# Kernel optimization log

Measured on AMD Instinct MI355X. Metric: run time of the kernel, lower is better.

The kernel has to match this reference:

```python
import jax, jax.numpy as jnp
import numpy as np
from jax import lax

B, LATENT, HIDDEN, N_STEPS = 2048, 256, 512, 100


def setup_inputs() -> dict:
    key = jax.random.key(0)
    ks = jax.random.split(key, 9)
    s_ih = 1.0 / np.sqrt(HIDDEN)
    return {
        "p0": jax.random.normal(ks[0], (B, LATENT), jnp.float32),
        "lat": jax.random.uniform(ks[1], (B,), jnp.float32, -1.0, 1.0),
        "lon": jax.random.uniform(ks[2], (B,), jnp.float32, -1.0, 1.0),
        "W_ih": jax.random.normal(ks[3], (3 * HIDDEN, LATENT + 2), jnp.float32) * s_ih,
        "W_hh": jax.random.normal(ks[4], (3 * HIDDEN, HIDDEN), jnp.float32) * s_ih,
        "b_ih": jax.random.normal(ks[5], (3 * HIDDEN,), jnp.float32) * s_ih,
        "b_hh": jax.random.normal(ks[6], (3 * HIDDEN,), jnp.float32) * s_ih,
        "W_proj": jax.random.normal(ks[7], (LATENT, HIDDEN), jnp.float32) * s_ih,
        "b_proj": jax.random.normal(ks[8], (LATENT,), jnp.float32) * s_ih,
        "n_steps": N_STEPS,
    }


def reference(p0, lat, lon, W_ih, W_hh, b_ih, b_hh, W_proj, b_proj, n_steps):
    H = W_hh.shape[1]
    ll = jnp.stack([lat, lon], axis=-1)  # (B, 2) conditioning, constant per step

    def step(carry, _):
        p, h = carry
        x = jnp.concatenate([p, ll], axis=-1)          # (B, latent+2)
        gi = x @ W_ih.T + b_ih                          # (B, 3H)
        gh = h @ W_hh.T + b_hh                          # (B, 3H)
        i_r, i_z, i_n = jnp.split(gi, 3, axis=-1)       # PyTorch gate order r,z,n
        h_r, h_z, h_n = jnp.split(gh, 3, axis=-1)
        r = jax.nn.sigmoid(i_r + h_r)
        z = jax.nn.sigmoid(i_z + h_z)
        n = jnp.tanh(i_n + r * h_n)
        h_new = (1.0 - z) * n + z * h
        p_new = h_new @ W_proj.T + b_proj               # (B, latent)
        return (p_new, h_new), p_new

    h0 = jnp.zeros((p0.shape[0], H), p0.dtype)
    _, ps = lax.scan(step, (p0, h0), None, length=n_steps)  # (T-1, B, latent)
    return jnp.concatenate([p0[None], ps], axis=0)          # (T, B, latent)
```

## Files before the change

kernel.cpp:

```cpp
#include <hip/hip_runtime.h>
#include <math.h>


#define B_SZ 2048
#define LAT  256
#define HID  512
#define NROW 2304
#define HN   (B_SZ * HID)

typedef unsigned short u16;
typedef __attribute__((ext_vector_type(4))) short s16x4;
typedef __attribute__((ext_vector_type(8))) short s16x8;
typedef __attribute__((ext_vector_type(4))) float f32x4;

__device__ __forceinline__ float sigm(float x) { return 1.0f / (1.0f + __expf(-x)); }
__device__ __forceinline__ float tanh_f(float x) {
    float e = __expf(-2.0f * fabsf(x));
    float t = (1.0f - e) / (1.0f + e);
    return copysignf(t, x);
}
__device__ __forceinline__ u16 f2bf(float x) {
    unsigned u = __float_as_uint(x);
    return (u16)((u + 0x7FFFu + ((u >> 16) & 1u)) >> 16);
}
__device__ __forceinline__ float bf2f(u16 h) { return __uint_as_float((unsigned)h << 16); }

__device__ __forceinline__ size_t fidx(int n, int k) {
    return ((size_t)(n >> 4) * 16 + (k >> 5)) * 512 +
           (size_t)((k >> 3) & 3) * 128 + (n & 15) * 8 + (k & 7);
}

__global__ __launch_bounds__(64) void k_bias(
    const float* __restrict__ W_ih, const float* __restrict__ b_ih,
    const float* __restrict__ b_hh, const float* __restrict__ b_pr,
    float* __restrict__ Bias)
{
    const int u = blockIdx.x;
    const int t = threadIdx.x;
    float dr = 0.f, dz = 0.f, dn = 0.f;
    for (int o = t; o < 256; o += 64) {
        float bo = b_pr[o];
        dr = fmaf(bo, W_ih[(size_t)u * 258 + o], dr);
        dz = fmaf(bo, W_ih[(size_t)(HID + u) * 258 + o], dz);
        dn = fmaf(bo, W_ih[(size_t)(2 * HID + u) * 258 + o], dn);
    }
    #pragma unroll
    for (int off = 32; off > 0; off >>= 1) {
        dr += __shfl_down(dr, off);
        dz += __shfl_down(dz, off);
        dn += __shfl_down(dn, off);
    }
    if (t == 0) {
        float* b = Bias + u * 12;
        b[0]  = b_ih[u] + b_hh[u] + dr;
        b[1]  = W_ih[(size_t)u * 258 + 256];
        b[2]  = W_ih[(size_t)u * 258 + 257];
        b[3]  = b_ih[HID + u] + b_hh[HID + u] + dz;
        b[4]  = W_ih[(size_t)(HID + u) * 258 + 256];
        b[5]  = W_ih[(size_t)(HID + u) * 258 + 257];
        b[6]  = b_ih[2 * HID + u] + dn;
        b[7]  = W_ih[(size_t)(2 * HID + u) * 258 + 256];
        b[8]  = W_ih[(size_t)(2 * HID + u) * 258 + 257];
        b[9]  = b_hh[2 * HID + u];
        b[10] = b_hh[u];
        b[11] = b_hh[HID + u];
    }
}

__global__ __launch_bounds__(512) void k_gi1(
    const float* __restrict__ p0, const float* __restrict__ latv,
    const float* __restrict__ lonv, const float* __restrict__ W_ih,
    const float* __restrict__ b_ih, float* __restrict__ gi1T,
    float* __restrict__ out)
{
    const int rb = blockIdx.x;
    const int t  = threadIdx.x;
    __shared__ float p0s[8][256];
    __shared__ float lat_s[8], lon_s[8];
    for (int i = t; i < 8 * 256; i += 512) {
        int r = i >> 8, o = i & 255;
        float v = p0[(size_t)(rb * 8 + r) * LAT + o];
        p0s[r][o] = v;
        out[(size_t)(rb * 8 + r) * LAT + o] = v;
    }
    if (t < 8) { lat_s[t] = latv[rb * 8 + t]; lon_s[t] = lonv[rb * 8 + t]; }
    __syncthreads();

    for (int gg = 0; gg < 3; ++gg) {
        const int grow = t + gg * 512;
        const float* wr = W_ih + (size_t)grow * 258;
        float acc[8];
        float bi = b_ih[grow];
        #pragma unroll
        for (int r = 0; r < 8; ++r) acc[r] = bi;
        for (int o = 0; o < 256; ++o) {
            float wv = wr[o];
            #pragma unroll
            for (int r = 0; r < 8; ++r) acc[r] = fmaf(wv, p0s[r][o], acc[r]);
        }
        float c1 = wr[256], c2 = wr[257];
        #pragma unroll
        for (int r = 0; r < 8; ++r) {
            acc[r] = fmaf(lat_s[r], c1, acc[r]);
            acc[r] = fmaf(lon_s[r], c2, acc[r]);
            gi1T[(size_t)grow * B_SZ + rb * 8 + r] = acc[r];
        }
    }
}

__global__ __launch_bounds__(256) void k_h1(
    const float* __restrict__ gi1T, const float* __restrict__ Bias,
    u16* __restrict__ Hhi, u16* __restrict__ Hlo)
{
    const int idx = blockIdx.x * 256 + threadIdx.x;
    const int row = idx & (B_SZ - 1);
    const int u   = idx >> 11;
    const float* bb = Bias + (size_t)u * 12;
    float r = sigm(gi1T[(size_t)u * B_SZ + row] + bb[10]);
    float z = sigm(gi1T[(size_t)(HID + u) * B_SZ + row] + bb[11]);
    float n = tanh_f(fmaf(r, bb[9], gi1T[(size_t)(2 * HID + u) * B_SZ + row]));
    float h = n - z * n;
    u16 hi = f2bf(h);
    size_t off = HN + fidx(row, u);
    Hhi[off] = hi;
    Hlo[off] = f2bf(h - bf2f(hi));
}

__global__ __launch_bounds__(512) void k_wsplit(
    const float* __restrict__ W_ih, const float* __restrict__ W_hh,
    const float* __restrict__ W_pr, u16* __restrict__ Whi, u16* __restrict__ Wlo)
{
    const int n = blockIdx.x;
    const int k = threadIdx.x;
    const int u = n >> 2, g = n & 3;
    __shared__ float wr[256];
    if (n < 2048 && g != 3 && k < 256)
        wr[k] = W_ih[(size_t)(g * HID + u) * 258 + k];
    __syncthreads();

    float w;
    if (n >= 2048) {
        w = W_pr[(size_t)(n - 2048) * HID + k];
    } else if (g == 3) {
        w = W_hh[(size_t)(2 * HID + u) * HID + k];
    } else {
        float acc = 0.f;
        for (int o = 0; o < 256; ++o)
            acc = fmaf(wr[o], W_pr[(size_t)o * HID + k], acc);
        if (g == 0)      acc += W_hh[(size_t)u * HID + k];
        else if (g == 1) acc += W_hh[(size_t)(HID + u) * HID + k];
        w = acc;
    }
    u16 hi = f2bf(w);
    size_t off = fidx(n, k);
    Whi[off] = hi;
    Wlo[off] = f2bf(w - bf2f(hi));
}

__global__ __launch_bounds__(256, 4) void k_gates(
    u16* __restrict__ Hhi, u16* __restrict__ Hlo,
    const u16* __restrict__ Whi,
    const float* __restrict__ Bias,
    const float* __restrict__ latv, const float* __restrict__ lonv,
    int sA, int sW, int ra, int rw)
{
    const int bid = blockIdx.x;
    const int xcd = bid & 7, loc = bid >> 3;
    const int mt  = (xcd & 3) * 8 + (loc & 7);
    const int nt  = (xcd >> 2) * 16 + (loc >> 3);
    const int m0  = mt * 64, n0 = nt * 64;
    const int t    = threadIdx.x;
    const int lane = t & 63, wave = t >> 6;
    const int wm   = wave >> 1, wn = wave & 1;
    const int q    = lane >> 4, c = lane & 15;

    __shared__ float Gt[64][68];
    __shared__ float bias_s[16][12];
    if (t < 192) ((float*)bias_s)[t] = Bias[(size_t)(n0 >> 2) * 12 + t];

    const u16* __restrict__ Hh = Hhi + (size_t)sA * HN;
    const u16* __restrict__ Hl = Hlo + (size_t)ra * HN;

    int aoff[2], boff[2];
    #pragma unroll
    for (int i = 0; i < 2; ++i)
        aoff[i] = ((mt * 4 + wm * 2 + i) * 16) * 512 + lane * 8;
    #pragma unroll
    for (int j = 0; j < 2; ++j)
        boff[j] = ((nt * 4 + wn * 2 + j) * 16) * 512 + lane * 8;

    f32x4 acc[2][2];
    #pragma unroll
    for (int i = 0; i < 2; ++i)
        #pragma unroll
        for (int j = 0; j < 2; ++j) acc[i][j] = (f32x4){0.f, 0.f, 0.f, 0.f};

    #pragma unroll 2
    for (int kb = 0; kb < 16; ++kb) {
        const int ko = kb * 512;
        s16x8 ah[2], bh[2];
        #pragma unroll
        for (int i = 0; i < 2; ++i)
            ah[i] = *(const s16x8*)(Hh + aoff[i] + ko);
        #pragma unroll
        for (int j = 0; j < 2; ++j)
            bh[j] = *(const s16x8*)(Whi + boff[j] + ko);
        #pragma unroll
        for (int i = 0; i < 2; ++i)
            #pragma unroll
            for (int j = 0; j < 2; ++j)
                acc[i][j] = __builtin_amdgcn_mfma_f32_16x16x32_bf16(ah[i], bh[j], acc[i][j], 0, 0, 0);
    }

    #pragma unroll
    for (int i = 0; i < 2; ++i)
        #pragma unroll
        for (int j = 0; j < 2; ++j)
            #pragma unroll
            for (int r = 0; r < 4; ++r)
                Gt[wm * 32 + i * 16 + 4 * q + r][wn * 32 + j * 16 + c] = acc[i][j][r];
    __syncthreads();

    u16* __restrict__ Hhn = Hhi + (size_t)sW * HN;
    u16* __restrict__ Hln = Hlo + (size_t)rw * HN;

    const int ug = t & 3;
    const int ml = t >> 2;
    const int m  = m0 + ml;
    const float lt = latv[m], ln = lonv[m];
    const size_t hoff = ((size_t)(m >> 4) * 16 + (nt >> 1)) * 512 +
                        (size_t)((nt & 1) * 2 + (ug >> 1)) * 128 +
                        (m & 15) * 8 + (ug & 1) * 4;
    s16x4 hh4 = *(const s16x4*)(Hh + hoff);
    s16x4 hl4 = *(const s16x4*)(Hl + hoff);
    s16x4 vh, vl;
    #pragma unroll
    for (int j = 0; j < 4; ++j) {
        const float* bb = bias_s[ug * 4 + j];
        f32x4 gv = *(const f32x4*)&Gt[ml][(ug * 4 + j) * 4];
        float r = sigm(gv.x + bb[0] + lt * bb[1] + ln * bb[2]);
        float z = sigm(gv.y + bb[3] + lt * bb[4] + ln * bb[5]);
        float n = tanh_f(fmaf(r, gv.w + bb[9], gv.z + bb[6] + lt * bb[7] + ln * bb[8]));
        float hold = bf2f((u16)hh4[j]) + bf2f((u16)hl4[j]);
        float h = n + z * (hold - n);
        u16 hi = f2bf(h);
        vh[j] = (short)hi;
        vl[j] = (short)f2bf(h - bf2f(hi));
    }
    *(s16x4*)(Hhn + hoff) = vh;
    *(s16x4*)(Hln + hoff) = vl;
}

__global__ __launch_bounds__(256, 2) void k_proj(
    const u16* __restrict__ Hhi, const u16* __restrict__ Whi,
    const float* __restrict__ b_pr, float* __restrict__ out)
{
    const int bid  = blockIdx.x;
    const int pt   = bid >> 1, ntp = bid & 1;
    const int slab = (pt >> 4) + 1;
    const int mt   = pt & 15;
    const int m0   = mt * 128;
    const int t    = threadIdx.x;
    const int lane = t & 63, wave = t >> 6;
    const int wm   = wave >> 1, wn = wave & 1;
    const int q    = lane >> 4, c = lane & 15;

    __shared__ float Gt[64][132];

    const u16* __restrict__ Hh = Hhi + (size_t)slab * HN;

    int aoff[4], boff[4];
    #pragma unroll
    for (int i = 0; i < 4; ++i) {
        aoff[i] = ((mt * 8 + wm * 4 + i) * 16) * 512 + lane * 8;
        boff[i] = ((128 + ntp * 8 + wn * 4 + i) * 16) * 512 + lane * 8;
    }

    f32x4 acc[4][4];
    #pragma unroll
    for (int i = 0; i < 4; ++i)
        #pragma unroll
        for (int j = 0; j < 4; ++j) acc[i][j] = (f32x4){0.f, 0.f, 0.f, 0.f};

    #pragma unroll 2
    for (int kb = 0; kb < 16; ++kb) {
        const int ko = kb * 512;
        s16x8 ah[4], bh[4];
        #pragma unroll
        for (int i = 0; i < 4; ++i) {
            ah[i] = *(const s16x8*)(Hh  + aoff[i] + ko);
            bh[i] = *(const s16x8*)(Whi + boff[i] + ko);
        }
        #pragma unroll
        for (int i = 0; i < 4; ++i)
            #pragma unroll
            for (int j = 0; j < 4; ++j)
                acc[i][j] = __builtin_amdgcn_mfma_f32_16x16x32_bf16(ah[i], bh[j], acc[i][j], 0, 0, 0);
    }

    for (int half = 0; half < 2; ++half) {
        __syncthreads();
        if (wm == half) {
            #pragma unroll
            for (int i = 0; i < 4; ++i)
                #pragma unroll
                for (int j = 0; j < 4; ++j)
                    #pragma unroll
                    for (int r = 0; r < 4; ++r)
                        Gt[i * 16 + 4 * q + r][wn * 64 + j * 16 + c] = acc[i][j][r];
        }
        __syncthreads();

        const int cl = t & 31, rg = t >> 5;
        const int o  = ntp * 128 + cl * 4;
        const float4 bp = *(const float4*)(b_pr + o);
        float* ob = out + (size_t)slab * B_SZ * LAT + o;
        #pragma unroll
        for (int i = 0; i < 8; ++i) {
            const int ml2 = rg * 8 + i;
            f32x4 g = *(const f32x4*)&Gt[ml2][cl * 4];
            *(float4*)(ob + (size_t)(m0 + half * 64 + ml2) * LAT) =
                make_float4(g.x + bp.x, g.y + bp.y, g.z + bp.z, g.w + bp.w);
        }
    }
}

__global__ __launch_bounds__(256) void k_gemm(
    u16* __restrict__ Hhi, u16* __restrict__ Hlo,
    const u16* __restrict__ Whi, const u16* __restrict__ Wlo,
    const float* __restrict__ Bias, const float* __restrict__ b_pr,
    const float* __restrict__ latv, const float* __restrict__ lonv,
    float* __restrict__ out, int s, int ns, int ntb, int ntc)
{
    const int bid  = blockIdx.x;
    const int nt   = ntb + bid % ntc;
    const int mt   = bid / ntc;
    const int m0   = mt * 128, n0 = nt * 128;
    const int t    = threadIdx.x;
    const int lane = t & 63, wave = t >> 6;
    const int wm   = wave >> 1, wn = wave & 1;
    const int q    = lane >> 4, c = lane & 15;

    __shared__ float Gt[64][132];
    __shared__ float bias_s[32][12];
    if (n0 < 2048) {
        for (int i = t; i < 384; i += 256)
            ((float*)bias_s)[i] = Bias[(size_t)(n0 >> 2) * 12 + i];
    }

    const u16* __restrict__ Hh = Hhi + (size_t)((s - 1) & 1) * HN;
    const u16* __restrict__ Hl = Hlo + (size_t)((s - 1) & 1) * HN;

    int aoff[4], boff[4];
    #pragma unroll
    for (int i = 0; i < 4; ++i) {
        aoff[i] = ((mt * 8 + wm * 4 + i) * 16) * 512 + lane * 8;
        boff[i] = ((nt * 8 + wn * 4 + i) * 16) * 512 + lane * 8;
    }

    f32x4 acc[4][4];
    #pragma unroll
    for (int i = 0; i < 4; ++i)
        #pragma unroll
        for (int j = 0; j < 4; ++j) acc[i][j] = (f32x4){0.f, 0.f, 0.f, 0.f};

    #pragma unroll 2
    for (int kb = 0; kb < 16; ++kb) {
        const int ko = kb * 512;
        s16x8 ah[4], al[4], bh[4], bl[4];
        #pragma unroll
        for (int i = 0; i < 4; ++i) {
            ah[i] = *(const s16x8*)(Hh  + aoff[i] + ko);
            al[i] = *(const s16x8*)(Hl  + aoff[i] + ko);
            bh[i] = *(const s16x8*)(Whi + boff[i] + ko);
            bl[i] = *(const s16x8*)(Wlo + boff[i] + ko);
        }
        #pragma unroll
        for (int i = 0; i < 4; ++i)
            #pragma unroll
            for (int j = 0; j < 4; ++j) {
                acc[i][j] = __builtin_amdgcn_mfma_f32_16x16x32_bf16(ah[i], bh[j], acc[i][j], 0, 0, 0);
                acc[i][j] = __builtin_amdgcn_mfma_f32_16x16x32_bf16(al[i], bh[j], acc[i][j], 0, 0, 0);
                acc[i][j] = __builtin_amdgcn_mfma_f32_16x16x32_bf16(ah[i], bl[j], acc[i][j], 0, 0, 0);
            }
    }

    u16* __restrict__ Hhn = Hhi + (size_t)(s & 1) * HN;
    u16* __restrict__ Hln = Hlo + (size_t)(s & 1) * HN;
    const int u0t = n0 >> 2;

    for (int half = 0; half < 2; ++half) {
        __syncthreads();
        if (wm == half) {
            #pragma unroll
            for (int i = 0; i < 4; ++i)
                #pragma unroll
                for (int j = 0; j < 4; ++j)
                    #pragma unroll
                    for (int r = 0; r < 4; ++r)
                        Gt[i * 16 + 4 * q + r][wn * 64 + j * 16 + c] = acc[i][j][r];
        }
        __syncthreads();

        if (n0 < 2048) {
            const int uo = t & 3;
            const int ml = t >> 2;
            const int m  = m0 + half * 64 + ml;
            const float lt = latv[m], ln = lonv[m];
            const size_t hoff = ((size_t)(m >> 4) * 16 + (u0t >> 5)) * 512 +
                                (size_t)uo * 128 + (m & 15) * 8;
            s16x8 hh8 = *(const s16x8*)(Hh + hoff);
            s16x8 hl8 = *(const s16x8*)(Hl + hoff);
            s16x8 vh, vl;
            #pragma unroll
            for (int j = 0; j < 8; ++j) {
                const float* bb = bias_s[uo * 8 + j];
                f32x4 gv = *(const f32x4*)&Gt[ml][(uo * 8 + j) * 4];
                float r = sigm(gv.x + bb[0] + lt * bb[1] + ln * bb[2]);
                float z = sigm(gv.y + bb[3] + lt * bb[4] + ln * bb[5]);
                float n = tanh_f(fmaf(r, gv.w + bb[9], gv.z + bb[6] + lt * bb[7] + ln * bb[8]));
                float hold = bf2f((u16)hh8[j]) + bf2f((u16)hl8[j]);
                float h = n + z * (hold - n);
                u16 hi = f2bf(h);
                vh[j] = (short)hi;
                vl[j] = (short)f2bf(h - bf2f(hi));
            }
            *(s16x8*)(Hhn + hoff) = vh;
            *(s16x8*)(Hln + hoff) = vl;
        } else {
            const int cl = t & 31, rg = t >> 5;
            const int o  = (n0 - 2048) + cl * 4;
            const float4 bp = *(const float4*)(b_pr + o);
            float* ob = out + (size_t)(s - 1) * B_SZ * LAT + o;
            #pragma unroll
            for (int i = 0; i < 8; ++i) {
                const int ml = rg * 8 + i;
                f32x4 g = *(const f32x4*)&Gt[ml][cl * 4];
                *(float4*)(ob + (size_t)(m0 + half * 64 + ml) * LAT) =
                    make_float4(g.x + bp.x, g.y + bp.y, g.z + bp.z, g.w + bp.w);
            }
        }
    }
}

extern "C" void kernel_launch(void* const* d_in, const int* in_sizes, int n_in,
                              void* d_out, int out_size, void* d_ws, size_t ws_size,
                              hipStream_t stream)
{
    const float* p0   = (const float*)d_in[0];
    const float* latv = (const float*)d_in[1];
    const float* lonv = (const float*)d_in[2];
    const float* W_ih = (const float*)d_in[3];
    const float* W_hh = (const float*)d_in[4];
    const float* b_ih = (const float*)d_in[5];
    const float* b_hh = (const float*)d_in[6];
    const float* W_pr = (const float*)d_in[7];
    const float* b_pr = (const float*)d_in[8];
    float* out = (float*)d_out;

    const int NS = out_size / (B_SZ * LAT) - 1;

    float* gi1T = (float*)d_ws;
    float* Bias = gi1T + 3 * HID * B_SZ;
    u16*   Whi  = (u16*)gi1T;
    u16*   Wlo  = Whi + (size_t)NROW * HID;

    const size_t offH     = ((size_t)3 * HID * B_SZ + 512 * 12) * sizeof(float);
    const size_t slabB    = (size_t)HN * sizeof(u16);
    const size_t needFast = offH + (size_t)(NS + 1) * slabB + 2 * slabB;
    const bool   fast     = ws_size >= needFast;
    const int    nslabHi  = fast ? (NS + 1) : 2;

    u16* Hhi = (u16*)((char*)d_ws + offH);
    u16* Hlo = Hhi + (size_t)nslabHi * HN;

    hipLaunchKernelGGL(k_bias,   dim3(HID),  dim3(64),  0, stream, W_ih, b_ih, b_hh, b_pr, Bias);
    hipLaunchKernelGGL(k_gi1,    dim3(256),  dim3(512), 0, stream, p0, latv, lonv, W_ih, b_ih, gi1T, out);
    hipLaunchKernelGGL(k_h1,     dim3(4096), dim3(256), 0, stream, gi1T, Bias, Hhi, Hlo);
    hipLaunchKernelGGL(k_wsplit, dim3(NROW), dim3(512), 0, stream, W_ih, W_hh, W_pr, Whi, Wlo);

    if (fast) {
        for (int s = 2; s <= NS; ++s) {
            hipLaunchKernelGGL(k_gates, dim3(1024), dim3(256), 0, stream,
                               Hhi, Hlo, Whi, Bias, latv, lonv,
                               s - 1, s, (s - 1) & 1, s & 1);
        }
        hipLaunchKernelGGL(k_proj, dim3(NS * 32), dim3(256), 0, stream,
                           Hhi, Whi, b_pr, out);
    } else {
        for (int s = 2; s <= NS + 1; ++s) {
            const int ntc = (s <= NS) ? 18 : 2;
            const int ntb = (s <= NS) ? 0 : 16;
            hipLaunchKernelGGL(k_gemm, dim3(16 * ntc), dim3(256), 0, stream,
                               Hhi, Hlo, Whi, Wlo, Bias, b_pr, latv, lonv, out, s, NS, ntb, ntc);
        }
    }
}
```

Baseline: 1.400 ms.

## Fuse per-step projection into gate kernel launches instead of trailing proj kernel

Adds 128 extra blocks to each per-step gate launch. They compute the projection of the previous hidden state and write it straight to the output, so the large batched k_proj launch shrinks to only the final slab. The intent is to run the projection work in the idle slots of the latency-bound recurrent step launches rather than in a separate serial kernel. In exchange, each step launch becomes larger and its projection blocks compete for CUs and bandwidth with the critical-path gate blocks.

Result: slower. 1.574 ms (+12.4%).

```diff
diff --git a/kernel.cpp b/kernel.cpp
--- a/kernel.cpp
+++ b/kernel.cpp
@@ -160,23 +160,34 @@
 __global__ __launch_bounds__(256, 4) void k_gates(
     u16* __restrict__ Hhi, u16* __restrict__ Hlo,
     const u16* __restrict__ Whi,
-    const float* __restrict__ Bias,
+    const float* __restrict__ Bias, const float* __restrict__ b_pr,
     const float* __restrict__ latv, const float* __restrict__ lonv,
+    float* __restrict__ out,
     int sA, int sW, int ra, int rw)
 {
     const int bid = blockIdx.x;
-    const int xcd = bid & 7, loc = bid >> 3;
-    const int mt  = (xcd & 3) * 8 + (loc & 7);
-    const int nt  = (xcd >> 2) * 16 + (loc >> 3);
-    const int m0  = mt * 64, n0 = nt * 64;
+    const bool isproj = bid >= 1024;
     const int t    = threadIdx.x;
     const int lane = t & 63, wave = t >> 6;
     const int wm   = wave >> 1, wn = wave & 1;
     const int q    = lane >> 4, c = lane & 15;
 
+    int mt, nt = 0, ntp = 0;
+    if (!isproj) {
+        const int xcd = bid & 7, loc = bid >> 3;
+        mt = (xcd & 3) * 8 + (loc & 7);
+        nt = (xcd >> 2) * 16 + (loc >> 3);
+    } else {
+        const int pt = bid - 1024;
+        mt  = pt >> 2;
+        ntp = pt & 3;
+    }
+    const int m0 = mt * 64;
+
     __shared__ float Gt[64][68];
     __shared__ float bias_s[16][12];
-    if (t < 192) ((float*)bias_s)[t] = Bias[(size_t)(n0 >> 2) * 12 + t];
+    if (!isproj && t < 192)
+        ((float*)bias_s)[t] = Bias[(size_t)(nt * 16) * 12 + t];
 
     const u16* __restrict__ Hh = Hhi + (size_t)sA * HN;
     const u16* __restrict__ Hl = Hlo + (size_t)ra * HN;
@@ -186,8 +197,11 @@
     for (int i = 0; i < 2; ++i)
         aoff[i] = ((mt * 4 + wm * 2 + i) * 16) * 512 + lane * 8;
     #pragma unroll
-    for (int j = 0; j < 2; ++j)
-        boff[j] = ((nt * 4 + wn * 2 + j) * 16) * 512 + lane * 8;
+    for (int j = 0; j < 2; ++j) {
+        const int rb = isproj ? (128 + ntp * 4 + wn * 2 + j)
+                              : (nt * 4 + wn * 2 + j);
+        boff[j] = (rb * 16) * 512 + lane * 8;
+    }
 
     f32x4 acc[2][2];
     #pragma unroll
@@ -221,43 +235,57 @@
                 Gt[wm * 32 + i * 16 + 4 * q + r][wn * 32 + j * 16 + c] = acc[i][j][r];
     __syncthreads();
 
-    u16* __restrict__ Hhn = Hhi + (size_t)sW * HN;
-    u16* __restrict__ Hln = Hlo + (size_t)rw * HN;
-
-    const int ug = t & 3;
-    const int ml = t >> 2;
-    const int m  = m0 + ml;
-    const float lt = latv[m], ln = lonv[m];
-    const size_t hoff = ((size_t)(m >> 4) * 16 + (nt >> 1)) * 512 +
-                        (size_t)((nt & 1) * 2 + (ug >> 1)) * 128 +
-                        (m & 15) * 8 + (ug & 1) * 4;
-    s16x4 hh4 = *(const s16x4*)(Hh + hoff);
-    s16x4 hl4 = *(const s16x4*)(Hl + hoff);
-    s16x4 vh, vl;
-    #pragma unroll
-    for (int j = 0; j < 4; ++j) {
-        const float* bb = bias_s[ug * 4 + j];
-        f32x4 gv = *(const f32x4*)&Gt[ml][(ug * 4 + j) * 4];
-        float r = sigm(gv.x + bb[0] + lt * bb[1] + ln * bb[2]);
-        float z = sigm(gv.y + bb[3] + lt * bb[4] + ln * bb[5]);
-        float n = tanh_f(fmaf(r, gv.w + bb[9], gv.z + bb[6] + lt * bb[7] + ln * bb[8]));
-        float hold = bf2f((u16)hh4[j]) + bf2f((u16)hl4[j]);
-        float h = n + z * (hold - n);
-        u16 hi = f2bf(h);
-        vh[j] = (short)hi;
-        vl[j] = (short)f2bf(h - bf2f(hi));
-    }
-    *(s16x4*)(Hhn + hoff) = vh;
-    *(s16x4*)(Hln + hoff) = vl;
+    if (!isproj) {
+        u16* __restrict__ Hhn = Hhi + (size_t)sW * HN;
+        u16* __restrict__ Hln = Hlo + (size_t)rw * HN;
+
+        const int ug = t & 3;
+        const int ml = t >> 2;
+        const int m  = m0 + ml;
+        const float lt = latv[m], ln = lonv[m];
+        const size_t hoff = ((size_t)(m >> 4) * 16 + (nt >> 1)) * 512 +
+                            (size_t)((nt & 1) * 2 + (ug >> 1)) * 128 +
+                            (m & 15) * 8 + (ug & 1) * 4;
+        s16x4 hh4 = *(const s16x4*)(Hh + hoff);
+        s16x4 hl4 = *(const s16x4*)(Hl + hoff);
+        s16x4 vh, vl;
+        #pragma unroll
+        for (int j = 0; j < 4; ++j) {
+            const float* bb = bias_s[ug * 4 + j];
+            f32x4 gv = *(const f32x4*)&Gt[ml][(ug * 4 + j) * 4];
+            float r = sigm(gv.x + bb[0] + lt * bb[1] + ln * bb[2]);
+            float z = sigm(gv.y + bb[3] + lt * bb[4] + ln * bb[5]);
+            float n = tanh_f(fmaf(r, gv.w + bb[9], gv.z + bb[6] + lt * bb[7] + ln * bb[8]));
+            float hold = bf2f((u16)hh4[j]) + bf2f((u16)hl4[j]);
+            float h = n + z * (hold - n);
+            u16 hi = f2bf(h);
+            vh[j] = (short)hi;
+            vl[j] = (short)f2bf(h - bf2f(hi));
+        }
+        *(s16x4*)(Hhn + hoff) = vh;
+        *(s16x4*)(Hln + hoff) = vl;
+    } else {
+        const int cl = t & 15, rg = t >> 4;
+        const int o  = ntp * 64 + cl * 4;
+        const float4 bp = *(const float4*)(b_pr + o);
+        float* ob = out + (size_t)sA * B_SZ * LAT + o;
+        #pragma unroll
+        for (int i = 0; i < 4; ++i) {
+            const int ml = i * 16 + rg;
+            f32x4 g = *(const f32x4*)&Gt[ml][cl * 4];
+            *(float4*)(ob + (size_t)(m0 + ml) * LAT) =
+                make_float4(g.x + bp.x, g.y + bp.y, g.z + bp.z, g.w + bp.w);
+        }
+    }
 }
 
 __global__ __launch_bounds__(256, 2) void k_proj(
     const u16* __restrict__ Hhi, const u16* __restrict__ Whi,
-    const float* __restrict__ b_pr, float* __restrict__ out)
+    const float* __restrict__ b_pr, float* __restrict__ out, int slab_base)
 {
     const int bid  = blockIdx.x;
     const int pt   = bid >> 1, ntp = bid & 1;
-    const int slab = (pt >> 4) + 1;
+    const int slab = slab_base + (pt >> 4);
     const int mt   = pt & 15;
     const int m0   = mt * 128;
     const int t    = threadIdx.x;
@@ -469,10 +497,10 @@
     const size_t slabB    = (size_t)HN * sizeof(u16);
     const size_t needFast = offH + (size_t)(NS + 1) * slabB + 2 * slabB;
     const bool   fast     = ws_size >= needFast;
-    const int    nslabHi  = fast ? (NS + 1) : 2;
+    const int    nsH      = fast ? (NS + 1) : 2;
 
     u16* Hhi = (u16*)((char*)d_ws + offH);
-    u16* Hlo = Hhi + (size_t)nslabHi * HN;
+    u16* Hlo = Hhi + (size_t)nsH * HN;
 
     hipLaunchKernelGGL(k_bias,   dim3(HID),  dim3(64),  0, stream, W_ih, b_ih, b_hh, b_pr, Bias);
     hipLaunchKernelGGL(k_gi1,    dim3(256),  dim3(512), 0, stream, p0, latv, lonv, W_ih, b_ih, gi1T, out);
@@ -481,12 +509,12 @@
 
     if (fast) {
         for (int s = 2; s <= NS; ++s) {
-            hipLaunchKernelGGL(k_gates, dim3(1024), dim3(256), 0, stream,
-                               Hhi, Hlo, Whi, Bias, latv, lonv,
+            hipLaunchKernelGGL(k_gates, dim3(1152), dim3(256), 0, stream,
+                               Hhi, Hlo, Whi, Bias, b_pr, latv, lonv, out,
                                s - 1, s, (s - 1) & 1, s & 1);
         }
-        hipLaunchKernelGGL(k_proj, dim3(NS * 32), dim3(256), 0, stream,
-                           Hhi, Whi, b_pr, out);
+        hipLaunchKernelGGL(k_proj, dim3(32), dim3(256), 0, stream,
+                           Hhi, Whi, b_pr, out, NS);
     } else {
         for (int s = 2; s <= NS + 1; ++s) {
             const int ntc = (s <= NS) ? 18 : 2;
```
